# Performance work log

Measured on AMD Instinct MI355X. Metric: run time of the kernel, lower is better.

The kernel has to match this reference:

```python
import jax, jax.numpy as jnp
import numpy as np

OFFSET = 1  # self.offset

def setup_inputs() -> dict:
    key = jax.random.key(0)
    k1, k2, k3, k4, k5 = jax.random.split(key, 5)
    B, D, T, S, N = 16, 512, 1024, 12, 10
    x = jax.random.normal(k1, (B, D, T), dtype=jnp.float32)
    y = jax.random.normal(k2, (B, D, T), dtype=jnp.float32)
    W = jax.random.normal(k3, (D, D, S), dtype=jnp.float32) * 0.05  # ConvTranspose2d weight [in, out, 1, steps] squeezed
    b = jax.random.normal(k4, (D,), dtype=jnp.float32) * 0.05
    neg_idxs = jax.random.randint(k5, (B, N * T), 0, T)
    return {"x": x, "y": y, "W": W, "b": b, "neg_idxs": neg_idxs}


def reference(x, y, W, b, neg_idxs):
    B, F, T = y.shape
    N = neg_idxs.shape[1] // T
    # --- sample_negatives: gather by computed index over flattened y ---
    y_flat = jnp.transpose(y, (1, 0, 2)).reshape(F, B * T)          # [F, B*T]
    idx = (neg_idxs + jnp.arange(B, dtype=neg_idxs.dtype)[:, None] * T).reshape(-1)
    negs = y_flat[:, idx].reshape(F, B, N, T).transpose(2, 1, 0, 3)  # [N, B, F, T]
    targets = jnp.concatenate([y[None], negs], axis=0)               # [C=N+1, B, F, T]
    # --- project_to_steps: ConvTranspose2d with kernel (1, steps) == per-step linear ---
    xp = jnp.einsum('bit,ios->bots', x, W) + b[None, :, None, None]  # [B, F, T, S]
    C = N + 1
    S = xp.shape[-1]
    steps = min(S, T - OFFSET)
    preds, labels = [], []
    for i in range(steps):  # small fixed loop over prediction steps
        off = i + OFFSET
        # [C, B, T-off]: dot over feature dim, copies broadcast over x
        p = jnp.einsum('bft,cbft->cbt', xp[:, :, :T - off, i], targets[:, :, :, off:])
        preds.append(p.reshape(-1))
        lab = jnp.zeros((C, B * (T - off)), dtype=xp.dtype).at[0].set(1.0)
        labels.append(lab.reshape(-1))
    predictions = jnp.concatenate(preds)
    labels_out = jnp.concatenate(labels)
    return predictions, labels_out
```

## Files before the change

kernel.cpp:

```cpp
#include <hip/hip_runtime.h>

typedef __bf16 bf16x8 __attribute__((ext_vector_type(8)));
typedef float f32x4 __attribute__((ext_vector_type(4)));

#define B_ 16
#define T_ 1024
#define D_ 512
#define S_ 12
#define C_ 11
static constexpr int P_TOTAL = 2148960;

__device__ __host__ inline constexpr int pred_base(int i) {
  return C_ * B_ * (T_ * i - (i * (i + 1)) / 2);
}

__device__ inline unsigned short f2bf(float f) {
  unsigned int u = __float_as_uint(f);
  u += 0x7FFF + ((u >> 16) & 1);
  return (unsigned short)(u >> 16);
}

__device__ inline void gld16(const void* g, void* l) {
  __builtin_amdgcn_global_load_lds(
      (const __attribute__((address_space(1))) void*)g,
      (__attribute__((address_space(3))) void*)l, 16, 0, 0);
}

__global__ __launch_bounds__(256) void prep_w(const float* __restrict__ W,
                                              unsigned short* __restrict__ wt) {
  __shared__ unsigned short tile[32][33][12];
  const int i0 = blockIdx.x * 32, o0 = blockIdx.y * 32;
#pragma unroll
  for (int q = 0; q < 48; ++q) {
    int idx = threadIdx.x + q * 256;
    int ii = idx / 384, rem = idx % 384;
    int oo = rem / 12, ss = rem % 12;
    tile[ii][oo][ss] = f2bf(W[(size_t)(i0 + ii) * 6144 + (size_t)o0 * 12 + rem]);
  }
  __syncthreads();
#pragma unroll
  for (int q = 0; q < 48; ++q) {
    int idx = threadIdx.x + q * 256;
    int ss = idx / 1024, rem = idx % 1024;
    int oo = rem / 32, ii = rem % 32;
    wt[(size_t)ss * (D_ * D_) + (size_t)(o0 + oo) * D_ + (i0 + ii)] = tile[ii][oo][ss];
  }
}

__global__ __launch_bounds__(256) void prep_t(const float* __restrict__ in,
                                              unsigned short* __restrict__ ob) {
  __shared__ float tile[32][33];
  const int t0 = blockIdx.x * 32;
  const int d0 = blockIdx.y * 32;
  const int b = blockIdx.z;
  const float* ib = in + (size_t)b * D_ * T_;
  const int r = threadIdx.x / 32, c = threadIdx.x % 32;
#pragma unroll
  for (int p = 0; p < 4; ++p) {
    int rr = r + p * 8;
    tile[rr][c] = ib[(size_t)(d0 + rr) * T_ + t0 + c];
  }
  __syncthreads();
  unsigned short* op = ob + (size_t)b * T_ * D_;
#pragma unroll
  for (int p = 0; p < 4; ++p) {
    int rr = r + p * 8;
    op[(size_t)(t0 + rr) * D_ + d0 + c] = f2bf(tile[c][rr]);
  }
}

__global__ void labels_k(float* __restrict__ lab) {
  int k = blockIdx.x * 256 + threadIdx.x;
  if (k >= P_TOTAL) return;
  int i = 0;
#pragma unroll
  for (int q = 1; q < 12; ++q)
    if (k >= pred_base(q)) i = q;
  int rel = k - pred_base(i);
  int len = T_ - 1 - i;
  lab[k] = (rel < B_ * len) ? 1.0f : 0.0f;
}

__global__ __launch_bounds__(256) void gemm_xp(
    const unsigned short* __restrict__ xb,
    const unsigned short* __restrict__ wt,
    const float* __restrict__ bias,
    unsigned short* __restrict__ xp,
    int m0_global) {
  __shared__ unsigned short lA[2][128 * 32];
  __shared__ unsigned short lB[2][128 * 32];
  const int tid = threadIdx.x;
  const int s = blockIdx.z;
  const int n0 = blockIdx.y * 128;
  const int ml0 = blockIdx.x * 128;
  const unsigned short* Ag = xb + (size_t)(m0_global + ml0) * D_;
  const unsigned short* Bg = wt + ((size_t)s * D_ + n0) * D_;

  auto stage = [&](int buf, int kt) {
#pragma unroll
    for (int q = 0; q < 2; ++q) {
      int o2 = tid * 16 + q * 4096;
      int row = o2 >> 6;
      int colb = o2 & 63;
      gld16((const char*)Ag + (size_t)row * (D_ * 2) + kt * 64 + colb,
            (char*)(&lA[buf][0]) + o2);
      gld16((const char*)Bg + (size_t)row * (D_ * 2) + kt * 64 + colb,
            (char*)(&lB[buf][0]) + o2);
    }
  };

  const int w = tid >> 6, l = tid & 63;
  const int wm = (w >> 1) * 64, wn = (w & 1) * 64;
  const int fr = l & 15, koff = (l >> 4) * 8;

  f32x4 acc[4][4];
#pragma unroll
  for (int ia = 0; ia < 4; ++ia)
#pragma unroll
    for (int ib = 0; ib < 4; ++ib)
#pragma unroll
      for (int e = 0; e < 4; ++e) acc[ia][ib][e] = 0.f;

  stage(0, 0);
  asm volatile("s_waitcnt vmcnt(0)" ::: "memory");
  __syncthreads();

  for (int kt = 0; kt < 16; ++kt) {
    int cur = kt & 1;
    if (kt + 1 < 16) stage(cur ^ 1, kt + 1);
    bf16x8 af[4], bfr[4];
#pragma unroll
    for (int fm = 0; fm < 4; ++fm)
      af[fm] = *(const bf16x8*)&lA[cur][(wm + fm * 16 + fr) * 32 + koff];
#pragma unroll
    for (int fn = 0; fn < 4; ++fn)
      bfr[fn] = *(const bf16x8*)&lB[cur][(wn + fn * 16 + fr) * 32 + koff];
#pragma unroll
    for (int fm = 0; fm < 4; ++fm)
#pragma unroll
      for (int fn = 0; fn < 4; ++fn)
        acc[fm][fn] = __builtin_amdgcn_mfma_f32_16x16x32_bf16(
            af[fm], bfr[fn], acc[fm][fn], 0, 0, 0);
    asm volatile("s_waitcnt vmcnt(0)" ::: "memory");
    __syncthreads();
  }

  float bv[4];
#pragma unroll
  for (int fn = 0; fn < 4; ++fn) bv[fn] = bias[n0 + wn + fn * 16 + fr];

#pragma unroll
  for (int fm = 0; fm < 4; ++fm) {
#pragma unroll
    for (int r = 0; r < 4; ++r) {
      int m = ml0 + wm + fm * 16 + (l >> 4) * 4 + r;
      int bl = m >> 10, t = m & 1023;
      size_t orow = (((size_t)bl * S_ + s) * T_ + t) * D_;
#pragma unroll
      for (int fn = 0; fn < 4; ++fn) {
        int o = n0 + wn + fn * 16 + fr;
        xp[orow + o] = f2bf(acc[fm][fn][r] + bv[fn]);
      }
    }
  }
}

__global__ __launch_bounds__(256) void pred_k(
    const unsigned short* __restrict__ xp,
    const unsigned short* __restrict__ yT,
    const int* __restrict__ negs,
    float* __restrict__ preds, int b0) {
  const int w = threadIdx.x >> 6, l = threadIdx.x & 63;
  const int tt = blockIdx.x * 4 + w;
  const int bl = blockIdx.y;
  const int b = b0 + bl;
  if (tt < 1 || tt >= T_) return;

  const int fr = l & 15;
  const int koff = (l >> 4) * 8;

  int t = tt - 1 - fr;
  bool av = (fr < S_) && (t >= 0);
  int si = av ? fr : 0;
  int st = av ? t : 0;
  const unsigned short* arow = xp + (((size_t)bl * S_ + si) * T_ + st) * D_;

  int j = tt;
  if (fr >= 1 && fr <= 10) j = negs[b * (10 * T_) + (fr - 1) * T_ + tt];
  const unsigned short* brow = yT + ((size_t)b * T_ + j) * D_;

  f32x4 acc;
#pragma unroll
  for (int e = 0; e < 4; ++e) acc[e] = 0.f;
#pragma unroll
  for (int kk = 0; kk < 16; ++kk) {
    bf16x8 a = *(const bf16x8*)(arow + kk * 32 + koff);
    bf16x8 bb = *(const bf16x8*)(brow + kk * 32 + koff);
    acc = __builtin_amdgcn_mfma_f32_16x16x32_bf16(a, bb, acc, 0, 0, 0);
  }
#pragma unroll
  for (int r = 0; r < 4; ++r) {
    int ii = (l >> 4) * 4 + r;
    int to = tt - 1 - ii;
    if (ii < S_ && fr < C_ && to >= 0) {
      int len = T_ - 1 - ii;
      preds[pred_base(ii) + ((size_t)fr * B_ + b) * len + to] = acc[r];
    }
  }
}

extern "C" void kernel_launch(void* const* d_in, const int* in_sizes, int n_in,
                              void* d_out, int out_size, void* d_ws, size_t ws_size,
                              hipStream_t stream) {
  (void)in_sizes; (void)n_in; (void)out_size;
  const float* x = (const float*)d_in[0];
  const float* y = (const float*)d_in[1];
  const float* W = (const float*)d_in[2];
  const float* bias = (const float*)d_in[3];
  const int* negs = (const int*)d_in[4];
  float* out = (float*)d_out;
  char* ws = (char*)d_ws;

  unsigned short* wt = (unsigned short*)ws;
  unsigned short* xb = (unsigned short*)(ws + 6291456);
  unsigned short* yT = (unsigned short*)(ws + 6291456 + 16777216);
  unsigned short* xp = (unsigned short*)(ws + 6291456 + 2 * 16777216);
  const size_t fixed = 6291456 + (size_t)2 * 16777216;
  const size_t xp_per_b = (size_t)S_ * T_ * D_ * 2;
  int nb = 1;
  if (ws_size > fixed) {
    size_t cap = (ws_size - fixed) / xp_per_b;
    nb = cap < 1 ? 1 : (cap > 16 ? 16 : (int)cap);
  }

  hipLaunchKernelGGL(prep_w, dim3(16, 16), dim3(256), 0, stream, W, wt);
  hipLaunchKernelGGL(prep_t, dim3(32, 16, 16), dim3(256), 0, stream, x, xb);
  hipLaunchKernelGGL(prep_t, dim3(32, 16, 16), dim3(256), 0, stream, y, yT);
  hipLaunchKernelGGL(labels_k, dim3((P_TOTAL + 255) / 256), dim3(256), 0, stream,
                     out + P_TOTAL);

  for (int b0 = 0; b0 < B_; b0 += nb) {
    int bc = (B_ - b0) < nb ? (B_ - b0) : nb;
    hipLaunchKernelGGL(gemm_xp, dim3(bc * 8, 4, 12), dim3(256), 0, stream,
                       xb, wt, bias, xp, b0 * T_);
    hipLaunchKernelGGL(pred_k, dim3(256, bc), dim3(256), 0, stream,
                       xp, yT, negs, out, b0);
  }
}
```

Measured before the change: 233.4 us.

## Restructure xp GEMM into 256x256 tiles with 4-stage LDS pipeline and swizzle

Rewrites the projection GEMM to use 512-thread blocks computing 256x256 output tiles with 8 waves. Global-to-LDS loads now run two K-steps ahead through a four-buffer ring, the LDS layout is XOR-swizzled to avoid bank conflicts, and setprio raises MFMA priority. The goal is to hide load latency and raise MFMA utilization. In exchange the block count drops sharply (from 384 to 96 per batch chunk at full nb), which may leave CUs idle, and register pressure rises.

```diff
diff --git a/kernel.cpp b/kernel.cpp
--- a/kernel.cpp
+++ b/kernel.cpp
@@ -34,8 +34,8 @@
   for (int q = 0; q < 48; ++q) {
     int idx = threadIdx.x + q * 256;
     int ii = idx / 384, rem = idx % 384;
-    int oo = rem / 12, ss = rem % 12;
-    tile[ii][oo][ss] = f2bf(W[(size_t)(i0 + ii) * 6144 + (size_t)o0 * 12 + rem]);
+    tile[ii][rem / 12][rem % 12] =
+        f2bf(W[(size_t)(i0 + ii) * 6144 + (size_t)o0 * 12 + rem]);
   }
   __syncthreads();
 #pragma unroll
@@ -81,85 +81,120 @@
   lab[k] = (rel < B_ * len) ? 1.0f : 0.0f;
 }
 
-__global__ __launch_bounds__(256) void gemm_xp(
+__global__ __launch_bounds__(512, 2) void gemm_xp(
     const unsigned short* __restrict__ xb,
     const unsigned short* __restrict__ wt,
     const float* __restrict__ bias,
     unsigned short* __restrict__ xp,
     int m0_global) {
-  __shared__ unsigned short lA[2][128 * 32];
-  __shared__ unsigned short lB[2][128 * 32];
+  __shared__ unsigned short lds[65536];
   const int tid = threadIdx.x;
   const int s = blockIdx.z;
-  const int n0 = blockIdx.y * 128;
-  const int ml0 = blockIdx.x * 128;
+  const int n0 = blockIdx.y * 256;
+  const int ml0 = blockIdx.x * 256;
   const unsigned short* Ag = xb + (size_t)(m0_global + ml0) * D_;
   const unsigned short* Bg = wt + ((size_t)s * D_ + n0) * D_;
 
-  auto stage = [&](int buf, int kt) {
-#pragma unroll
-    for (int q = 0; q < 2; ++q) {
-      int o2 = tid * 16 + q * 4096;
-      int row = o2 >> 6;
-      int colb = o2 & 63;
-      gld16((const char*)Ag + (size_t)row * (D_ * 2) + kt * 64 + colb,
-            (char*)(&lA[buf][0]) + o2);
-      gld16((const char*)Bg + (size_t)row * (D_ * 2) + kt * 64 + colb,
-            (char*)(&lB[buf][0]) + o2);
+  auto stage = [&](const unsigned short* src, int kt, int regionShorts) {
+#pragma unroll
+    for (int h = 0; h < 2; ++h) {
+      int o = tid * 16 + h * 8192;
+      int row = o >> 6;
+      int sc = (o >> 4) & 3;
+      int lcol = (sc ^ ((row >> 1) & 3)) << 4;
+      gld16((const char*)src + (size_t)row * (D_ * 2) + kt * 64 + lcol,
+            (char*)&lds[regionShorts] + o);
     }
   };
 
   const int w = tid >> 6, l = tid & 63;
-  const int wm = (w >> 1) * 64, wn = (w & 1) * 64;
-  const int fr = l & 15, koff = (l >> 4) * 8;
-
-  f32x4 acc[4][4];
-#pragma unroll
-  for (int ia = 0; ia < 4; ++ia)
-#pragma unroll
-    for (int ib = 0; ib < 4; ++ib)
-#pragma unroll
-      for (int e = 0; e < 4; ++e) acc[ia][ib][e] = 0.f;
-
-  stage(0, 0);
-  asm volatile("s_waitcnt vmcnt(0)" ::: "memory");
-  __syncthreads();
+  const int gm = w >> 2, gn = w & 3;
+  const int fr = l & 15, sgrp = l >> 4;
+
+  auto rdfrag = [&](const unsigned short* base, int row) -> bf16x8 {
+    int idx = row * 32 + ((sgrp ^ ((row >> 1) & 3)) << 3);
+    return *(const bf16x8*)&base[idx];
+  };
+
+  f32x4 acc[2][4][4];
+#pragma unroll
+  for (int ms = 0; ms < 2; ++ms)
+#pragma unroll
+    for (int fm = 0; fm < 4; ++fm)
+#pragma unroll
+      for (int fn = 0; fn < 4; ++fn)
+#pragma unroll
+        for (int e = 0; e < 4; ++e) acc[ms][fm][fn][e] = 0.f;
+
+  stage(Ag, 0, 0);
+  stage(Bg, 0, 8192);
+  stage(Ag, 1, 16384);
+  stage(Bg, 1, 16384 + 8192);
+  asm volatile("s_waitcnt vmcnt(4)" ::: "memory");
+  __builtin_amdgcn_s_barrier();
 
   for (int kt = 0; kt < 16; ++kt) {
-    int cur = kt & 1;
-    if (kt + 1 < 16) stage(cur ^ 1, kt + 1);
-    bf16x8 af[4], bfr[4];
-#pragma unroll
-    for (int fm = 0; fm < 4; ++fm)
-      af[fm] = *(const bf16x8*)&lA[cur][(wm + fm * 16 + fr) * 32 + koff];
+    const unsigned short* A_l = &lds[(kt & 3) * 16384];
+    const unsigned short* B_l = A_l + 8192;
+    bf16x8 afrag[4], bfrag[4];
+
 #pragma unroll
     for (int fn = 0; fn < 4; ++fn)
-      bfr[fn] = *(const bf16x8*)&lB[cur][(wn + fn * 16 + fr) * 32 + koff];
+      bfrag[fn] = rdfrag(B_l, gn * 64 + fn * 16 + fr);
+#pragma unroll
+    for (int fm = 0; fm < 4; ++fm)
+      afrag[fm] = rdfrag(A_l, gm * 128 + fm * 16 + fr);
+    if (kt + 2 < 16) stage(Ag, kt + 2, ((kt + 2) & 3) * 16384);
+    __builtin_amdgcn_s_barrier();
+    __builtin_amdgcn_s_setprio(1);
 #pragma unroll
     for (int fm = 0; fm < 4; ++fm)
 #pragma unroll
       for (int fn = 0; fn < 4; ++fn)
-        acc[fm][fn] = __builtin_amdgcn_mfma_f32_16x16x32_bf16(
-            af[fm], bfr[fn], acc[fm][fn], 0, 0, 0);
-    asm volatile("s_waitcnt vmcnt(0)" ::: "memory");
-    __syncthreads();
+        acc[0][fm][fn] = __builtin_amdgcn_mfma_f32_16x16x32_bf16(
+            afrag[fm], bfrag[fn], acc[0][fm][fn], 0, 0, 0);
+    __builtin_amdgcn_s_setprio(0);
+    __builtin_amdgcn_s_barrier();
+
+#pragma unroll
+    for (int fm = 0; fm < 4; ++fm)
+      afrag[fm] = rdfrag(A_l, gm * 128 + 64 + fm * 16 + fr);
+    if (kt + 2 < 16) stage(Bg, kt + 2, ((kt + 2) & 3) * 16384 + 8192);
+    __builtin_amdgcn_s_barrier();
+    __builtin_amdgcn_s_setprio(1);
+#pragma unroll
+    for (int fm = 0; fm < 4; ++fm)
+#pragma unroll
+      for (int fn = 0; fn < 4; ++fn)
+        acc[1][fm][fn] = __builtin_amdgcn_mfma_f32_16x16x32_bf16(
+            afrag[fm], bfrag[fn], acc[1][fm][fn], 0, 0, 0);
+    __builtin_amdgcn_s_setprio(0);
+    if (kt <= 13) {
+      asm volatile("s_waitcnt vmcnt(4)" ::: "memory");
+    } else if (kt == 14) {
+      asm volatile("s_waitcnt vmcnt(0)" ::: "memory");
+    }
+    __builtin_amdgcn_s_barrier();
   }
 
   float bv[4];
 #pragma unroll
-  for (int fn = 0; fn < 4; ++fn) bv[fn] = bias[n0 + wn + fn * 16 + fr];
-
-#pragma unroll
-  for (int fm = 0; fm < 4; ++fm) {
-#pragma unroll
-    for (int r = 0; r < 4; ++r) {
-      int m = ml0 + wm + fm * 16 + (l >> 4) * 4 + r;
-      int bl = m >> 10, t = m & 1023;
-      size_t orow = (((size_t)bl * S_ + s) * T_ + t) * D_;
-#pragma unroll
-      for (int fn = 0; fn < 4; ++fn) {
-        int o = n0 + wn + fn * 16 + fr;
-        xp[orow + o] = f2bf(acc[fm][fn][r] + bv[fn]);
+  for (int fn = 0; fn < 4; ++fn) bv[fn] = bias[n0 + gn * 64 + fn * 16 + fr];
+
+#pragma unroll
+  for (int ms = 0; ms < 2; ++ms) {
+#pragma unroll
+    for (int fm = 0; fm < 4; ++fm) {
+#pragma unroll
+      for (int r = 0; r < 4; ++r) {
+        int m = ml0 + gm * 128 + ms * 64 + fm * 16 + (l >> 4) * 4 + r;
+        int bl = m >> 10, t = m & 1023;
+        size_t orow = (((size_t)bl * S_ + s) * T_ + t) * D_;
+#pragma unroll
+        for (int fn = 0; fn < 4; ++fn) {
+          int o = n0 + gn * 64 + fn * 16 + fr;
+          xp[orow + o] = f2bf(acc[ms][fm][fn][r] + bv[fn]);
+        }
       }
     }
   }
@@ -241,7 +276,7 @@
 
   for (int b0 = 0; b0 < B_; b0 += nb) {
     int bc = (B_ - b0) < nb ? (B_ - b0) : nb;
-    hipLaunchKernelGGL(gemm_xp, dim3(bc * 8, 4, 12), dim3(256), 0, stream,
+    hipLaunchKernelGGL(gemm_xp, dim3(bc * 4, 2, 12), dim3(512), 0, stream,
                        xb, wt, bias, xp, b0 * T_);
     hipLaunchKernelGGL(pred_k, dim3(256, bc), dim3(256), 0, stream,
                        xp, yT, negs, out, b0);
```

Result: faster. 223.4 us (-4.3%).
